# Kernel optimization log

Hardware: AMD Instinct MI355X
Metric: run time of the kernel (lower is better)

The kernel has to match this reference:

```python
import jax, jax.numpy as jnp
import numpy as np

# ---- static config (mirrors __init__ args) ----
IH, IW = 256, 704          # image_size
FH, FW = 32, 88            # feature_size
DBOUND = (1.0, 60.0, 0.5)  # -> D = 118
DX = jnp.array([0.3, 0.3, 20.0], jnp.float32)       # voxel size
BX = jnp.array([-53.85, -53.85, 0.0], jnp.float32)  # voxel-center offset (bound0 + dx/2)
NX, NY, NZ = 360, 360, 1
C_OUT = 80


def _frustum():
    ds = jnp.arange(*DBOUND, dtype=jnp.float32)          # [D]
    D = ds.shape[0]
    xs = jnp.linspace(0.0, IW - 1.0, FW, dtype=jnp.float32)
    ys = jnp.linspace(0.0, IH - 1.0, FH, dtype=jnp.float32)
    ds_g = jnp.broadcast_to(ds[:, None, None], (D, FH, FW))
    xs_g = jnp.broadcast_to(xs[None, None, :], (D, FH, FW))
    ys_g = jnp.broadcast_to(ys[None, :, None], (D, FH, FW))
    return jnp.stack([xs_g, ys_g, ds_g], axis=-1)        # [D, fH, fW, 3]


def setup_inputs() -> dict:
    key = jax.random.key(0)
    B, N, D = 1, 6, 118
    kx, kt = jax.random.split(key)
    x = jax.random.normal(kx, (B, N, D, FH, FW, C_OUT), jnp.float32)
    # camera frame (x right, y down, z fwd) -> lidar frame (x fwd, y left, z up)
    R = jnp.array([[0.0, 0.0, 1.0], [-1.0, 0.0, 0.0], [0.0, -1.0, 0.0]], jnp.float32)
    camera2lidar_rots = jnp.broadcast_to(R, (B, N, 3, 3)).copy()
    camera2lidar_trans = 0.5 * jax.random.normal(kt, (B, N, 3), jnp.float32)
    K = jnp.array([[600.0, 0.0, 352.0], [0.0, 600.0, 128.0], [0.0, 0.0, 1.0]], jnp.float32)
    intrins = jnp.broadcast_to(K, (B, N, 3, 3)).copy()
    post_rots = jnp.broadcast_to(jnp.eye(3, dtype=jnp.float32), (B, N, 3, 3)).copy()
    post_trans = jnp.zeros((B, N, 3), jnp.float32)
    extra_rots = jnp.broadcast_to(jnp.eye(3, dtype=jnp.float32), (B, 3, 3)).copy()
    extra_trans = jnp.zeros((B, 3), jnp.float32)
    return {
        "x": x,
        "camera2lidar_rots": camera2lidar_rots,
        "camera2lidar_trans": camera2lidar_trans,
        "intrins": intrins,
        "post_rots": post_rots,
        "post_trans": post_trans,
        "extra_rots": extra_rots,
        "extra_trans": extra_trans,
    }


def _get_geometry(c2l_rots, c2l_trans, intrins, post_rots, post_trans,
                  extra_rots, extra_trans):
    # points: [B, N, D, fH, fW, 3] in lidar coords
    frustum = _frustum()
    pts = frustum[None, None] - post_trans[:, :, None, None, None, :]
    inv_pr = jnp.linalg.inv(post_rots)                              # [B,N,3,3]
    pts = jnp.einsum('bnij,bndhwj->bndhwi', inv_pr, pts)
    # undo perspective: (u*d, v*d, d)
    pts = jnp.concatenate([pts[..., :2] * pts[..., 2:3], pts[..., 2:3]], axis=-1)
    combine = jnp.einsum('bnij,bnjk->bnik', c2l_rots, jnp.linalg.inv(intrins))
    pts = jnp.einsum('bnij,bndhwj->bndhwi', combine, pts)
    pts = pts + c2l_trans[:, :, None, None, None, :]
    pts = jnp.einsum('bij,bndhwj->bndhwi', extra_rots, pts)
    pts = pts + extra_trans[:, None, None, None, None, :]
    return pts


def _bev_pool(geom, x):
    B, N, D, H, W, C = x.shape
    Np = N * D * H * W
    # voxelize (torch .long() truncates toward zero; jnp int cast matches)
    coords = ((geom - (BX - DX / 2.0)) / DX).astype(jnp.int32)      # [B,N,D,H,W,3]
    coords = coords.reshape(B, Np, 3)
    cx, cy, cz = coords[..., 0], coords[..., 1], coords[..., 2]
    kept = (cx >= 0) & (cx < NX) & (cy >= 0) & (cy < NY) & (cz >= 0) & (cz < NZ)
    bidx = jnp.arange(B, dtype=jnp.int32)[:, None]
    flat = (((bidx * NZ + cz) * NX + cx) * NY + cy)                 # [B, Np]
    sentinel = B * NZ * NX * NY
    flat = jnp.where(kept, flat, sentinel)
    feats = x.reshape(B * Np, C)
    pooled = jax.ops.segment_sum(feats, flat.reshape(-1),
                                 num_segments=sentinel + 1)[:-1]    # drop invalid bin
    final = pooled.reshape(B, NZ, NX, NY, C)
    # -> [B, C, Z, X, Y] then cat over Z: [B, C*Z, X, Y]
    final = final.transpose(0, 4, 1, 2, 3).reshape(B, C * NZ, NX, NY)
    return final


def reference(x, camera2lidar_rots, camera2lidar_trans, intrins, post_rots,
              post_trans, extra_rots, extra_trans):
    geom = _get_geometry(camera2lidar_rots, camera2lidar_trans, intrins,
                         post_rots, post_trans, extra_rots, extra_trans)
    return _bev_pool(geom, x)
```

## Files before the change

### kernel.cpp

```cpp
#include <hip/hip_runtime.h>

#define NCAM 6
#define DN   118
#define FHH  32
#define FWW  88
#define CCH  80
#define NXV  360
#define NYV  360
#define NXY  (NXV*NYV)
#define ACC_BYTES ((size_t)NXY * CCH * 4)

typedef float f32x4 __attribute__((ext_vector_type(4)));

__device__ __forceinline__ void inv3_f64_to_f32(const float* a, float* inv) {
#pragma clang fp contract(off)
  double m00=a[0], m01=a[1], m02=a[2];
  double m10=a[3], m11=a[4], m12=a[5];
  double m20=a[6], m21=a[7], m22=a[8];
  double c00 = m11*m22 - m12*m21;
  double c01 = m10*m22 - m12*m20;
  double c02 = m10*m21 - m11*m20;
  double det = m00*c00 - m01*c01 + m02*c02;
  inv[0] = (float)( c00/det);
  inv[1] = (float)(-(m01*m22 - m02*m21)/det);
  inv[2] = (float)( (m01*m12 - m02*m11)/det);
  inv[3] = (float)(-c01/det);
  inv[4] = (float)( (m00*m22 - m02*m20)/det);
  inv[5] = (float)(-(m00*m12 - m02*m10)/det);
  inv[6] = (float)( c02/det);
  inv[7] = (float)(-(m00*m21 - m01*m20)/det);
  inv[8] = (float)( (m00*m11 - m01*m10)/det);
}

__global__ void setup_mats_kernel(const float* __restrict__ c2l_rots,
                                  const float* __restrict__ c2l_trans,
                                  const float* __restrict__ intrins,
                                  const float* __restrict__ post_rots,
                                  const float* __restrict__ post_trans,
                                  float* __restrict__ mats) {
#pragma clang fp contract(off)
  int n = threadIdx.x;
  if (n >= NCAM) return;
  float iPR[9], iK[9];
  inv3_f64_to_f32(post_rots + n*9, iPR);
  inv3_f64_to_f32(intrins  + n*9, iK);
  const float* R = c2l_rots + n*9;
  float* o = mats + n*24;
  for (int i = 0; i < 3; i++)
    for (int k = 0; k < 3; k++) {
      float s = R[i*3+0] * iK[0*3+k];
      s = s + R[i*3+1] * iK[1*3+k];
      s = s + R[i*3+2] * iK[2*3+k];
      o[9 + i*3 + k] = s;
    }
  for (int i = 0; i < 9; i++) o[i] = iPR[i];
  for (int i = 0; i < 3; i++) { o[18+i] = c2l_trans[n*3+i]; o[21+i] = post_trans[n*3+i]; }
}

template<bool DIRECT>
__device__ __forceinline__ void flush_acc(float* dst, int bin, int c, const float4& a) {
  if (DIRECT) {
    atomicAdd(dst + (size_t)(c+0)*NXY + bin, a.x);
    atomicAdd(dst + (size_t)(c+1)*NXY + bin, a.y);
    atomicAdd(dst + (size_t)(c+2)*NXY + bin, a.z);
    atomicAdd(dst + (size_t)(c+3)*NXY + bin, a.w);
  } else {
    float* p = dst + (size_t)bin*CCH + c;
    atomicAdd(p+0, a.x); atomicAdd(p+1, a.y);
    atomicAdd(p+2, a.z); atomicAdd(p+3, a.w);
  }
}

template<bool DIRECT>
__global__ __launch_bounds__(256) void scatter_kernel(
    const float* __restrict__ x,
    const float* __restrict__ mats,
    const float* __restrict__ extra_rots,
    const float* __restrict__ extra_trans,
    float* __restrict__ dst) {
#pragma clang fp contract(off)
  __shared__ int bins[256];
  const int b  = blockIdx.x;
  const int nd = b / (FWW/8);
  const int w0 = (b - nd*(FWW/8)) * 8;
  const int n  = nd / DN;
  const int d  = nd - n*DN;
  const int t  = threadIdx.x;

  {
    const int wl = t >> 5, h = t & 31;
    const int w  = w0 + wl;
    const float* M = mats + n*24;
    float u   = (float)(((double)w * 703.0) / 87.0);
    float v   = (float)(((double)h * 255.0) / 31.0);
    float dep = 1.0f + 0.5f*(float)d;
    float f0 = u - M[21], f1 = v - M[22], f2 = dep - M[23];
    float s;
    s = M[0]*f0; s = s + M[1]*f1; s = s + M[2]*f2; float g0 = s;
    s = M[3]*f0; s = s + M[4]*f1; s = s + M[5]*f2; float g1 = s;
    s = M[6]*f0; s = s + M[7]*f1; s = s + M[8]*f2; float g2 = s;
    float q0 = g0*g2, q1 = g1*g2, q2 = g2;
    s = M[ 9]*q0; s = s + M[10]*q1; s = s + M[11]*q2; float r0 = s + M[18];
    s = M[12]*q0; s = s + M[13]*q1; s = s + M[14]*q2; float r1 = s + M[19];
    s = M[15]*q0; s = s + M[16]*q1; s = s + M[17]*q2; float r2 = s + M[20];
    s = extra_rots[0]*r0; s = s + extra_rots[1]*r1; s = s + extra_rots[2]*r2; float e0 = s + extra_trans[0];
    s = extra_rots[3]*r0; s = s + extra_rots[4]*r1; s = s + extra_rots[5]*r2; float e1 = s + extra_trans[1];
    s = extra_rots[6]*r0; s = s + extra_rots[7]*r1; s = s + extra_rots[8]*r2; float e2 = s + extra_trans[2];
    const float bs01 = -53.85f - (0.3f*0.5f);
    const float bs2  =   0.0f  - (20.0f*0.5f);
    float fx = (e0 - bs01) / 0.3f;
    float fy = (e1 - bs01) / 0.3f;
    float fz = (e2 - bs2 ) / 20.0f;
    int cx = (int)fx, cy = (int)fy, cz = (int)fz;
    bool kept = (cx >= 0) & (cx < NXV) & (cy >= 0) & (cy < NYV) & (cz >= 0) & (cz < 1);
    bins[t] = kept ? ((cz*NXV + cx)*NYV + cy) : -1;
  }
  __syncthreads();

  if (t < 160) {
    const int wl = t / 20, c4 = (t - wl*20) * 4;
    const int w  = w0 + wl;
    const float* xb = x + (((size_t)nd*FHH*FWW + w) * CCH + c4);
    const int* bl = bins + (wl << 5);

    unsigned mask = 0u;
    int bin0 = -1;
    bool uniform = true;
#pragma unroll
    for (int h = 0; h < FHH; h++) {
      int bi = bl[h];
      if (bi >= 0) {
        if (bin0 < 0)           bin0 = bi;
        else if (bi != bin0)    uniform = false;
        mask |= (1u << h);
      }
    }

    if (uniform) {
      if (mask != 0u) {
        float4 acc = make_float4(0.f, 0.f, 0.f, 0.f);
#pragma unroll
        for (int h = 0; h < FHH; h++) {
          const f32x4 v = __builtin_nontemporal_load(
              (const f32x4*)(xb + (size_t)h * (FWW*CCH)));
          const bool k = (mask >> h) & 1u;
          acc.x += k ? v.x : 0.0f;
          acc.y += k ? v.y : 0.0f;
          acc.z += k ? v.z : 0.0f;
          acc.w += k ? v.w : 0.0f;
        }
        flush_acc<DIRECT>(dst, bin0, c4, acc);
      }
    } else {
      float4 acc = make_float4(0.f, 0.f, 0.f, 0.f);
      int cur = -1;
      for (int h = 0; h < FHH; h++) {
        int bi = bl[h];
        if (bi != cur) {
          if (cur >= 0) flush_acc<DIRECT>(dst, cur, c4, acc);
          cur = bi;
          acc = make_float4(0.f, 0.f, 0.f, 0.f);
        }
        if (bi >= 0) {
          const float4 val = *(const float4*)(xb + (size_t)h * (FWW*CCH));
          acc.x += val.x; acc.y += val.y; acc.z += val.z; acc.w += val.w;
        }
      }
      if (cur >= 0) flush_acc<DIRECT>(dst, cur, c4, acc);
    }
  }
}

__global__ __launch_bounds__(256) void transpose_kernel(const float* __restrict__ accum,
                                                        float* __restrict__ out) {
  __shared__ float tile[64*81];
  const int xy0 = blockIdx.x * 64;
  const int t = threadIdx.x;
  for (int i = t; i < 64*CCH; i += 256) {
    int r = i / CCH, c = i - r*CCH;
    tile[r*81 + c] = accum[(size_t)(xy0 + r)*CCH + c];
  }
  __syncthreads();
  for (int i = t; i < 64*CCH; i += 256) {
    int c = i >> 6, r = i & 63;
    out[(size_t)c*NXY + xy0 + r] = tile[r*81 + c];
  }
}

extern "C" void kernel_launch(void* const* d_in, const int* in_sizes, int n_in,
                              void* d_out, int out_size, void* d_ws, size_t ws_size,
                              hipStream_t stream) {
  const float* x           = (const float*)d_in[0];
  const float* c2l_rots    = (const float*)d_in[1];
  const float* c2l_trans   = (const float*)d_in[2];
  const float* intrins     = (const float*)d_in[3];
  const float* post_rots   = (const float*)d_in[4];
  const float* post_trans  = (const float*)d_in[5];
  const float* extra_rots  = (const float*)d_in[6];
  const float* extra_trans = (const float*)d_in[7];
  float* out = (float*)d_out;
  const int nblocks = NCAM * DN * (FWW/8);

  if (ws_size >= ACC_BYTES + 1024) {
    float* accum = (float*)d_ws;
    float* mats  = (float*)((char*)d_ws + ACC_BYTES);
    hipMemsetAsync(accum, 0, ACC_BYTES, stream);
    setup_mats_kernel<<<1, 64, 0, stream>>>(c2l_rots, c2l_trans, intrins,
                                            post_rots, post_trans, mats);
    scatter_kernel<false><<<nblocks, 256, 0, stream>>>(x, mats, extra_rots,
                                                       extra_trans, accum);
    transpose_kernel<<<NXY/64, 256, 0, stream>>>(accum, out);
  } else {
    float* mats = (float*)d_ws;
    hipMemsetAsync(out, 0, (size_t)out_size * 4, stream);
    setup_mats_kernel<<<1, 64, 0, stream>>>(c2l_rots, c2l_trans, intrins,
                                            post_rots, post_trans, mats);
    scatter_kernel<true><<<nblocks, 256, 0, stream>>>(x, mats, extra_rots,
                                                      extra_trans, out);
  }
}
```

Baseline: 820.5 us.

## Split bin computation into separate kernel and reduce with full-thread tasks

Geometry and bin computation moves into its own kernel that writes per-point bins to workspace. A new reduce kernel maps every thread to a (w, channel-quad) task, reading the 32 bins of its column with vector loads, so all 256 threads do reduction work instead of 160 with a shared-memory barrier. This adds an extra kernel launch and a global bins buffer round trip. The workspace requirement grows, so if the workspace is too small the code falls back to the direct path.

```diff
diff --git a/kernel.cpp b/kernel.cpp
--- a/kernel.cpp
+++ b/kernel.cpp
@@ -9,6 +9,10 @@
 #define NYV  360
 #define NXY  (NXV*NYV)
 #define ACC_BYTES ((size_t)NXY * CCH * 4)
+#define NPTS   (NCAM*DN*FHH*FWW)
+#define BINS_BYTES ((size_t)NPTS * 4)
+#define TASKS_PER_ND (FWW*(CCH/4))
+#define CHUNKS 7
 
 typedef float f32x4 __attribute__((ext_vector_type(4)));
 
@@ -57,6 +61,54 @@
   for (int i = 0; i < 3; i++) { o[18+i] = c2l_trans[n*3+i]; o[21+i] = post_trans[n*3+i]; }
 }
 
+__device__ __forceinline__ int point_bin(int n, int d, int h, int w,
+                                         const float* __restrict__ mats,
+                                         const float* __restrict__ extra_rots,
+                                         const float* __restrict__ extra_trans) {
+#pragma clang fp contract(off)
+  const float* M = mats + n*24;
+  float u   = (float)(((double)w * 703.0) / 87.0);
+  float v   = (float)(((double)h * 255.0) / 31.0);
+  float dep = 1.0f + 0.5f*(float)d;
+  float f0 = u - M[21], f1 = v - M[22], f2 = dep - M[23];
+  float s;
+  s = M[0]*f0; s = s + M[1]*f1; s = s + M[2]*f2; float g0 = s;
+  s = M[3]*f0; s = s + M[4]*f1; s = s + M[5]*f2; float g1 = s;
+  s = M[6]*f0; s = s + M[7]*f1; s = s + M[8]*f2; float g2 = s;
+  float q0 = g0*g2, q1 = g1*g2, q2 = g2;
+  s = M[ 9]*q0; s = s + M[10]*q1; s = s + M[11]*q2; float r0 = s + M[18];
+  s = M[12]*q0; s = s + M[13]*q1; s = s + M[14]*q2; float r1 = s + M[19];
+  s = M[15]*q0; s = s + M[16]*q1; s = s + M[17]*q2; float r2 = s + M[20];
+  s = extra_rots[0]*r0; s = s + extra_rots[1]*r1; s = s + extra_rots[2]*r2; float e0 = s + extra_trans[0];
+  s = extra_rots[3]*r0; s = s + extra_rots[4]*r1; s = s + extra_rots[5]*r2; float e1 = s + extra_trans[1];
+  s = extra_rots[6]*r0; s = s + extra_rots[7]*r1; s = s + extra_rots[8]*r2; float e2 = s + extra_trans[2];
+  const float bs01 = -53.85f - (0.3f*0.5f);
+  const float bs2  =   0.0f  - (20.0f*0.5f);
+  float fx = (e0 - bs01) / 0.3f;
+  float fy = (e1 - bs01) / 0.3f;
+  float fz = (e2 - bs2 ) / 20.0f;
+  int cx = (int)fx, cy = (int)fy, cz = (int)fz;
+  bool kept = (cx >= 0) & (cx < NXV) & (cy >= 0) & (cy < NYV) & (cz >= 0) & (cz < 1);
+  return kept ? ((cz*NXV + cx)*NYV + cy) : -1;
+}
+
+__global__ __launch_bounds__(256) void bins_kernel(
+    const float* __restrict__ mats,
+    const float* __restrict__ extra_rots,
+    const float* __restrict__ extra_trans,
+    int* __restrict__ bins_g) {
+  const int b  = blockIdx.x;
+  const int nd = b / (FWW/8);
+  const int w0 = (b - nd*(FWW/8)) * 8;
+  const int n  = nd / DN;
+  const int d  = nd - n*DN;
+  const int t  = threadIdx.x;
+  const int wl = t >> 5, h = t & 31;
+  const int w  = w0 + wl;
+  bins_g[((size_t)nd*FWW + w)*FHH + h] =
+      point_bin(n, d, h, w, mats, extra_rots, extra_trans);
+}
+
 template<bool DIRECT>
 __device__ __forceinline__ void flush_acc(float* dst, int bin, int c, const float4& a) {
   if (DIRECT) {
@@ -71,14 +123,85 @@
   }
 }
 
-template<bool DIRECT>
-__global__ __launch_bounds__(256) void scatter_kernel(
+__global__ __launch_bounds__(256) void reduce_kernel(
+    const float* __restrict__ x,
+    const int* __restrict__ bins_g,
+    float* __restrict__ dst) {
+  const int bid = blockIdx.x;
+  const int nd  = bid / CHUNKS;
+  const int task = (bid - nd*CHUNKS) * 256 + threadIdx.x;
+  if (task >= TASKS_PER_ND) return;
+  const int w  = task / 20;
+  const int c4 = (task - w*20) * 4;
+
+  const int4* bg = (const int4*)(bins_g + ((size_t)nd*FWW + w)*FHH);
+  int col[FHH];
+  {
+    int4 q[8];
+#pragma unroll
+    for (int i = 0; i < 8; i++) q[i] = bg[i];
+#pragma unroll
+    for (int i = 0; i < 8; i++) {
+      col[4*i+0] = q[i].x; col[4*i+1] = q[i].y;
+      col[4*i+2] = q[i].z; col[4*i+3] = q[i].w;
+    }
+  }
+
+  unsigned mask = 0u;
+  int bin0 = -1;
+  bool uniform = true;
+#pragma unroll
+  for (int h = 0; h < FHH; h++) {
+    int bi = col[h];
+    if (bi >= 0) {
+      if (bin0 < 0)        bin0 = bi;
+      else if (bi != bin0) uniform = false;
+      mask |= (1u << h);
+    }
+  }
+  if (mask == 0u) return;
+
+  const float* xb = x + ((size_t)nd*FHH*FWW + w) * CCH + c4;
+
+  if (uniform) {
+    float4 acc = make_float4(0.f, 0.f, 0.f, 0.f);
+#pragma unroll
+    for (int h = 0; h < FHH; h++) {
+      const f32x4 v = __builtin_nontemporal_load(
+          (const f32x4*)(xb + (size_t)h * (FWW*CCH)));
+      const bool k = (mask >> h) & 1u;
+      acc.x += k ? v.x : 0.0f;
+      acc.y += k ? v.y : 0.0f;
+      acc.z += k ? v.z : 0.0f;
+      acc.w += k ? v.w : 0.0f;
+    }
+    flush_acc<false>(dst, bin0, c4, acc);
+  } else {
+    float4 acc = make_float4(0.f, 0.f, 0.f, 0.f);
+    int cur = -1;
+#pragma unroll
+    for (int h = 0; h < FHH; h++) {
+      int bi = col[h];
+      if (bi != cur) {
+        if (cur >= 0) flush_acc<false>(dst, cur, c4, acc);
+        cur = bi;
+        acc = make_float4(0.f, 0.f, 0.f, 0.f);
+      }
+      if (bi >= 0) {
+        const float4 val = *(const float4*)(xb + (size_t)h * (FWW*CCH));
+        acc.x += val.x; acc.y += val.y; acc.z += val.z; acc.w += val.w;
+      }
+    }
+    if (cur >= 0) flush_acc<false>(dst, cur, c4, acc);
+  }
+}
+
+__global__ __launch_bounds__(256) void scatter_direct_kernel(
     const float* __restrict__ x,
     const float* __restrict__ mats,
     const float* __restrict__ extra_rots,
     const float* __restrict__ extra_trans,
     float* __restrict__ dst) {
-#pragma clang fp contract(off)
   __shared__ int bins[256];
   const int b  = blockIdx.x;
   const int nd = b / (FWW/8);
@@ -86,88 +209,31 @@
   const int n  = nd / DN;
   const int d  = nd - n*DN;
   const int t  = threadIdx.x;
-
   {
     const int wl = t >> 5, h = t & 31;
-    const int w  = w0 + wl;
-    const float* M = mats + n*24;
-    float u   = (float)(((double)w * 703.0) / 87.0);
-    float v   = (float)(((double)h * 255.0) / 31.0);
-    float dep = 1.0f + 0.5f*(float)d;
-    float f0 = u - M[21], f1 = v - M[22], f2 = dep - M[23];
-    float s;
-    s = M[0]*f0; s = s + M[1]*f1; s = s + M[2]*f2; float g0 = s;
-    s = M[3]*f0; s = s + M[4]*f1; s = s + M[5]*f2; float g1 = s;
-    s = M[6]*f0; s = s + M[7]*f1; s = s + M[8]*f2; float g2 = s;
-    float q0 = g0*g2, q1 = g1*g2, q2 = g2;
-    s = M[ 9]*q0; s = s + M[10]*q1; s = s + M[11]*q2; float r0 = s + M[18];
-    s = M[12]*q0; s = s + M[13]*q1; s = s + M[14]*q2; float r1 = s + M[19];
-    s = M[15]*q0; s = s + M[16]*q1; s = s + M[17]*q2; float r2 = s + M[20];
-    s = extra_rots[0]*r0; s = s + extra_rots[1]*r1; s = s + extra_rots[2]*r2; float e0 = s + extra_trans[0];
-    s = extra_rots[3]*r0; s = s + extra_rots[4]*r1; s = s + extra_rots[5]*r2; float e1 = s + extra_trans[1];
-    s = extra_rots[6]*r0; s = s + extra_rots[7]*r1; s = s + extra_rots[8]*r2; float e2 = s + extra_trans[2];
-    const float bs01 = -53.85f - (0.3f*0.5f);
-    const float bs2  =   0.0f  - (20.0f*0.5f);
-    float fx = (e0 - bs01) / 0.3f;
-    float fy = (e1 - bs01) / 0.3f;
-    float fz = (e2 - bs2 ) / 20.0f;
-    int cx = (int)fx, cy = (int)fy, cz = (int)fz;
-    bool kept = (cx >= 0) & (cx < NXV) & (cy >= 0) & (cy < NYV) & (cz >= 0) & (cz < 1);
-    bins[t] = kept ? ((cz*NXV + cx)*NYV + cy) : -1;
+    bins[t] = point_bin(n, d, h, w0 + wl, mats, extra_rots, extra_trans);
   }
   __syncthreads();
-
   if (t < 160) {
     const int wl = t / 20, c4 = (t - wl*20) * 4;
     const int w  = w0 + wl;
     const float* xb = x + (((size_t)nd*FHH*FWW + w) * CCH + c4);
     const int* bl = bins + (wl << 5);
-
-    unsigned mask = 0u;
-    int bin0 = -1;
-    bool uniform = true;
-#pragma unroll
+    float4 acc = make_float4(0.f, 0.f, 0.f, 0.f);
+    int cur = -1;
     for (int h = 0; h < FHH; h++) {
       int bi = bl[h];
+      if (bi != cur) {
+        if (cur >= 0) flush_acc<true>(dst, cur, c4, acc);
+        cur = bi;
+        acc = make_float4(0.f, 0.f, 0.f, 0.f);
+      }
       if (bi >= 0) {
-        if (bin0 < 0)           bin0 = bi;
-        else if (bi != bin0)    uniform = false;
-        mask |= (1u << h);
-      }
-    }
-
-    if (uniform) {
-      if (mask != 0u) {
-        float4 acc = make_float4(0.f, 0.f, 0.f, 0.f);
-#pragma unroll
-        for (int h = 0; h < FHH; h++) {
-          const f32x4 v = __builtin_nontemporal_load(
-              (const f32x4*)(xb + (size_t)h * (FWW*CCH)));
-          const bool k = (mask >> h) & 1u;
-          acc.x += k ? v.x : 0.0f;
-          acc.y += k ? v.y : 0.0f;
-          acc.z += k ? v.z : 0.0f;
-          acc.w += k ? v.w : 0.0f;
-        }
-        flush_acc<DIRECT>(dst, bin0, c4, acc);
-      }
-    } else {
-      float4 acc = make_float4(0.f, 0.f, 0.f, 0.f);
-      int cur = -1;
-      for (int h = 0; h < FHH; h++) {
-        int bi = bl[h];
-        if (bi != cur) {
-          if (cur >= 0) flush_acc<DIRECT>(dst, cur, c4, acc);
-          cur = bi;
-          acc = make_float4(0.f, 0.f, 0.f, 0.f);
-        }
-        if (bi >= 0) {
-          const float4 val = *(const float4*)(xb + (size_t)h * (FWW*CCH));
-          acc.x += val.x; acc.y += val.y; acc.z += val.z; acc.w += val.w;
-        }
-      }
-      if (cur >= 0) flush_acc<DIRECT>(dst, cur, c4, acc);
-    }
+        const float4 val = *(const float4*)(xb + (size_t)h * (FWW*CCH));
+        acc.x += val.x; acc.y += val.y; acc.z += val.z; acc.w += val.w;
+      }
+    }
+    if (cur >= 0) flush_acc<true>(dst, cur, c4, acc);
   }
 }
 
@@ -199,23 +265,24 @@
   const float* extra_rots  = (const float*)d_in[6];
   const float* extra_trans = (const float*)d_in[7];
   float* out = (float*)d_out;
-  const int nblocks = NCAM * DN * (FWW/8);
-
-  if (ws_size >= ACC_BYTES + 1024) {
-    float* accum = (float*)d_ws;
-    float* mats  = (float*)((char*)d_ws + ACC_BYTES);
+  const int nb_pts = NCAM * DN * (FWW/8);
+
+  if (ws_size >= ACC_BYTES + 1024 + BINS_BYTES) {
+    float* accum  = (float*)d_ws;
+    float* mats   = (float*)((char*)d_ws + ACC_BYTES);
+    int*   bins_g = (int*)  ((char*)d_ws + ACC_BYTES + 1024);
     hipMemsetAsync(accum, 0, ACC_BYTES, stream);
     setup_mats_kernel<<<1, 64, 0, stream>>>(c2l_rots, c2l_trans, intrins,
                                             post_rots, post_trans, mats);
-    scatter_kernel<false><<<nblocks, 256, 0, stream>>>(x, mats, extra_rots,
-                                                       extra_trans, accum);
+    bins_kernel<<<nb_pts, 256, 0, stream>>>(mats, extra_rots, extra_trans, bins_g);
+    reduce_kernel<<<NCAM*DN*CHUNKS, 256, 0, stream>>>(x, bins_g, accum);
     transpose_kernel<<<NXY/64, 256, 0, stream>>>(accum, out);
   } else {
     float* mats = (float*)d_ws;
     hipMemsetAsync(out, 0, (size_t)out_size * 4, stream);
     setup_mats_kernel<<<1, 64, 0, stream>>>(c2l_rots, c2l_trans, intrins,
                                             post_rots, post_trans, mats);
-    scatter_kernel<true><<<nblocks, 256, 0, stream>>>(x, mats, extra_rots,
+    scatter_direct_kernel<<<nb_pts, 256, 0, stream>>>(x, mats, extra_rots,
                                                       extra_trans, out);
   }
 }
```

Measured after the change: 824.7 us. No clear change (+0.5%).
